# Kernel optimization log

Hardware: AMD Instinct MI355X
Metric: run time of the kernel (lower is better)

## Reference

```python
import jax, jax.numpy as jnp
import numpy as np

IN_DIMS = (32, 64, 96, 128)
N_EXPERTS = len(IN_DIMS)
MAX_F = max(IN_DIMS)
D = 2 * MAX_F
N = 8192
TOP_K = 2
H_DIM = 1024
OUT_DIM = 768
LN_EPS = 1e-6


def _build_mask():
    # mask[f] = [1]*s + [0]*(MAX_F-s) + [1]*s + [0]*(MAX_F-s), shape (E, 1, D)
    m = np.zeros((N_EXPERTS, 1, D), dtype=np.float32)
    for i, s in enumerate(IN_DIMS):
        m[i, 0, :s] = 1.0
        m[i, 0, MAX_F:MAX_F + s] = 1.0
    return jnp.asarray(m)

_MASK = _build_mask()


def _multi_in_expert(x_final, expert_weights, expert_indices, W, b):
    """MoE dispatch/combine of MultiInSizeLinear (expert_indices path).
    x_final: (E, N, D); expert_weights/indices: (N, K); W: (E, O, D); b: (E, O)."""
    Wm = W * _MASK                                   # (E, O, D) masked per-size weights
    # per-expert outputs for every token (the torch loop computes these per mask group)
    Y = jnp.einsum('end,eod->eno', x_final, Wm) + b[:, None, :]   # (E, N, O)
    valid = expert_indices < N_EXPERTS               # (N, K) real-expert mask
    rsum = jnp.sum(expert_weights * valid, axis=-1, keepdims=True)
    rsum = jnp.where(rsum == 0, 1.0, rsum)
    wnorm = jnp.where(valid, expert_weights / rsum, 0.0)          # (N, K)
    safe = jnp.where(valid, expert_indices, 0)
    n_idx = jnp.arange(Y.shape[1])
    gathered = Y[safe, n_idx[:, None]]               # (N, K, O)
    return jnp.sum(wnorm[..., None] * gathered, axis=1)           # (N, O)


def setup_inputs() -> dict:
    key = jax.random.key(0)
    ks = jax.random.split(key, 12)
    s_hid = 1.0 / np.sqrt(D)
    s_out = 1.0 / np.sqrt(H_DIM)
    return {
        'x': jax.random.normal(ks[0], (N, D), jnp.float32),
        'in_feat_size': jax.random.randint(ks[1], (N,), 0, MAX_F, jnp.int64) if jax.config.jax_enable_x64 else jax.random.randint(ks[1], (N,), 0, MAX_F, jnp.int32),
        'expert_weights': jax.random.uniform(ks[2], (N, TOP_K), jnp.float32),
        'expert_indices': jax.random.randint(ks[3], (N, TOP_K), 0, 6, jnp.int32),
        'x_final': jax.random.normal(ks[4], (N_EXPERTS, N, D), jnp.float32),
        'W_hid': jax.random.normal(ks[5], (N_EXPERTS, H_DIM, D), jnp.float32) * s_hid,
        'b_hid': jax.random.normal(ks[6], (N_EXPERTS, H_DIM), jnp.float32) * s_hid,
        'W_out': jax.random.normal(ks[7], (OUT_DIM, H_DIM), jnp.float32) * s_out,
        'b_out': jax.random.normal(ks[8], (OUT_DIM,), jnp.float32) * s_out,
        'W_res': jax.random.normal(ks[9], (N_EXPERTS, OUT_DIM, D), jnp.float32) * s_hid,
        'b_res': jax.random.normal(ks[10], (N_EXPERTS, OUT_DIM), jnp.float32) * s_hid,
        'ln_w': jnp.ones((OUT_DIM,), jnp.float32),
    }


def reference(x, in_feat_size, expert_weights, expert_indices, x_final,
              W_hid, b_hid, W_out, b_out, W_res, b_res, ln_w):
    xf = jnp.nan_to_num(x_final, nan=0.0)
    hid = _multi_in_expert(xf, expert_weights, expert_indices, W_hid, b_hid)
    hid = jax.nn.gelu(hid, approximate=False)
    out = hid @ W_out.T + b_out                      # output_layer (dropout p=0 -> identity)
    res = _multi_in_expert(xf, expert_weights, expert_indices, W_res, b_res)
    out = out + res
    # T5LayerNorm (RMSNorm)
    var = jnp.mean(out * out, axis=-1, keepdims=True)
    return ln_w * (out * jax.lax.rsqrt(var + LN_EPS))
```

## Files before the change

kernel.cpp:

```cpp
#include <hip/hip_runtime.h>
#include <hip/hip_bf16.h>

#define TOKENS 8192
#define D_IN   256
#define HDIM   1024
#define ODIM   768
#define KPACK  704
#define NCHUNK 88

typedef short bf16x8 __attribute__((ext_vector_type(8)));
typedef float f32x4  __attribute__((ext_vector_type(4)));

static __device__ __forceinline__ ushort f2b(float f) {
    union { __hip_bfloat16 b; ushort u; } cv;
    cv.b = __float2bfloat16(f);
    return cv.u;
}
static __device__ __forceinline__ float b2f(ushort u) {
    union { ushort u; __hip_bfloat16 b; } cv;
    cv.u = u;
    return __bfloat162float(cv.b);
}

static __device__ __forceinline__ void chunk_map(int c8, int& e, int& d0) {
    int cc;
    if (c8 < 8)       { e = 0; cc = c8; }
    else if (c8 < 24) { e = 1; cc = c8 - 8; }
    else if (c8 < 48) { e = 2; cc = c8 - 24; }
    else              { e = 3; cc = c8 - 48; }
    int half = 4 * (e + 1);
    d0 = (cc < half) ? cc * 8 : 128 + (cc - half) * 8;
}

static __device__ __forceinline__ void stage16(const ushort* g, ushort* l) {
    __builtin_amdgcn_global_load_lds(
        (const __attribute__((address_space(1))) void*)g,
        (__attribute__((address_space(3))) void*)l, 16, 0, 0);
}

static __device__ __forceinline__ float gelu_f(float v) {
    float y = 0.7978845608f * v * (1.f + 0.044715f * v * v);
    return v - v / (__expf(2.f * y) + 1.f);
}

#define A_ITEMS  (TOKENS * NCHUNK)
#define B_ITEMS  (1792 * NCHUNK)
#define W_ITEMS  (768 * 128)
__global__ __launch_bounds__(256) void k_pack(
    const float* __restrict__ ew, const int* __restrict__ ei,
    const float* __restrict__ xf,
    const float* __restrict__ Whid, const float* __restrict__ bhid,
    const float* __restrict__ Wres, const float* __restrict__ bres,
    const float* __restrict__ Wout,
    ushort* __restrict__ Ap, ushort* __restrict__ Bp, ushort* __restrict__ Wb) {
    int gid = blockIdx.x * 256 + threadIdx.x;
    if (gid < A_ITEMS) {
        int n  = gid / NCHUNK;
        int c8 = gid - n * NCHUNK;
        int   i0 = ei[2 * n], i1 = ei[2 * n + 1];
        float w0 = ew[2 * n], w1 = ew[2 * n + 1];
        bool v0 = (unsigned)i0 < 4u, v1 = (unsigned)i1 < 4u;
        float rs = (v0 ? w0 : 0.f) + (v1 ? w1 : 0.f);
        if (rs == 0.f) rs = 1.f;
        float o0 = v0 ? w0 / rs : 0.f;
        float o1 = v1 ? w1 / rs : 0.f;
        ushort o[8] __attribute__((aligned(16))) = {0, 0, 0, 0, 0, 0, 0, 0};
        if (c8 < 80) {
            int e, d0;
            chunk_map(c8, e, d0);
            float w = ((v0 && i0 == e) ? o0 : 0.f) + ((v1 && i1 == e) ? o1 : 0.f);
            if (w != 0.f) {
                const float* s = xf + ((size_t)e * TOKENS + n) * D_IN + d0;
#pragma unroll
                for (int j = 0; j < 8; ++j) {
                    float v = s[j];
                    if (!(v == v)) v = 0.f;
                    o[j] = f2b(w * v);
                }
            }
        } else if (c8 == 80) {
#pragma unroll
            for (int j = 0; j < 4; ++j) {
                float m = ((v0 && i0 == j) ? o0 : 0.f) + ((v1 && i1 == j) ? o1 : 0.f);
                o[j] = f2b(m);
            }
        }
        *(uint4*)(Ap + (size_t)n * KPACK + c8 * 8) = *(const uint4*)o;
    } else if (gid < A_ITEMS + B_ITEMS) {
        int g2 = gid - A_ITEMS;
        int o_ = g2 / NCHUNK;
        int c8 = g2 - o_ * NCHUNK;
        ushort v[8] __attribute__((aligned(16))) = {0, 0, 0, 0, 0, 0, 0, 0};
        if (c8 < 80) {
            int e, d0;
            chunk_map(c8, e, d0);
            const float* s = (o_ < HDIM)
                ? Whid + ((size_t)e * HDIM + o_) * D_IN + d0
                : Wres + ((size_t)e * ODIM + (o_ - HDIM)) * D_IN + d0;
#pragma unroll
            for (int j = 0; j < 8; ++j) v[j] = f2b(s[j]);
        } else if (c8 == 80) {
#pragma unroll
            for (int j = 0; j < 4; ++j) {
                float b = (o_ < HDIM) ? bhid[j * HDIM + o_] : bres[j * ODIM + (o_ - HDIM)];
                v[j] = f2b(b);
            }
        }
        *(uint4*)(Bp + (size_t)o_ * KPACK + c8 * 8) = *(const uint4*)v;
    } else {
        int g3 = gid - A_ITEMS - B_ITEMS;
        const float* s = Wout + (size_t)g3 * 8;
        ushort v[8] __attribute__((aligned(16)));
#pragma unroll
        for (int j = 0; j < 8; ++j) v[j] = f2b(s[j]);
        *(uint4*)(Wb + (size_t)g3 * 8) = *(const uint4*)v;
    }
}

__global__ __launch_bounds__(256, 2) void k_gemm1(
    const ushort* __restrict__ A, const ushort* __restrict__ B,
    ushort* __restrict__ hidB, ushort* __restrict__ resb) {
    __shared__ __align__(16) ushort As[2][128 * 64];
    __shared__ __align__(16) ushort Bs[2][128 * 64];
    const int tid = threadIdx.x;
    const int lane = tid & 63, w = tid >> 6;
    const int wr = w >> 1, wc = w & 1;
    const int r = lane & 15, g = lane >> 4;
    const int sx = r & 7;

    int bid  = blockIdx.x;
    int widx = (bid & 7) * 112 + (bid >> 3);
    int bm = widx / 14, bn = widx - bm * 14;

    const int srow = tid >> 3;
    const int gc   = (tid & 7) ^ (srow & 7);
    const ushort* Ag = A + (size_t)(bm * 128 + srow) * KPACK + gc * 8;
    const ushort* Bg = B + (size_t)(bn * 128 + srow) * KPACK + gc * 8;
    const int ldst = (w * 8) * 64;

#define G1_STAGE(p, kt) do {                                            \
    _Pragma("unroll")                                                   \
    for (int i_ = 0; i_ < 4; ++i_) {                                    \
        stage16(Ag + (size_t)(i_ * 32) * KPACK + (kt), &As[p][ldst + i_ * 32 * 64]); \
        stage16(Bg + (size_t)(i_ * 32) * KPACK + (kt), &Bs[p][ldst + i_ * 32 * 64]); \
    } } while (0)

    G1_STAGE(0, 0);
    G1_STAGE(1, 64);

    f32x4 acc[4][4] = {};
    const int cA = (wr * 64 + r) * 64;
    const int cB = (wc * 64 + r) * 64;
    const int cs0 = ((0 * 4 + g) ^ sx) * 8;
    const int cs1 = ((1 * 4 + g) ^ sx) * 8;

    int cur = 0;
#pragma unroll
    for (int t = 0; t < 11; ++t) {
        if (t < 10) asm volatile("s_waitcnt vmcnt(8)" ::: "memory");
        else        asm volatile("s_waitcnt vmcnt(0)" ::: "memory");
        __builtin_amdgcn_s_barrier();
        const ushort* Ab = As[cur];
        const ushort* Bb = Bs[cur];
        bf16x8 a0[4], b0[4], a1[4], b1[4];
#pragma unroll
        for (int jj = 0; jj < 4; ++jj) {
            b0[jj] = *(const bf16x8*)&Bb[cB + jj * 16 * 64 + cs0];
            b1[jj] = *(const bf16x8*)&Bb[cB + jj * 16 * 64 + cs1];
        }
#pragma unroll
        for (int i = 0; i < 4; ++i) {
            a0[i] = *(const bf16x8*)&Ab[cA + i * 16 * 64 + cs0];
            a1[i] = *(const bf16x8*)&Ab[cA + i * 16 * 64 + cs1];
        }
        asm volatile("s_waitcnt lgkmcnt(0)" ::: "memory");
        __builtin_amdgcn_sched_barrier(0);
        __builtin_amdgcn_s_barrier();
        if (t + 2 < 11) G1_STAGE(cur, (t + 2) * 64);
        __builtin_amdgcn_s_setprio(1);
#pragma unroll
        for (int i = 0; i < 4; ++i)
#pragma unroll
            for (int jj = 0; jj < 4; ++jj)
                acc[i][jj] = __builtin_amdgcn_mfma_f32_16x16x32_bf16(
                    a0[i], b0[jj], acc[i][jj], 0, 0, 0);
#pragma unroll
        for (int i = 0; i < 4; ++i)
#pragma unroll
            for (int jj = 0; jj < 4; ++jj)
                acc[i][jj] = __builtin_amdgcn_mfma_f32_16x16x32_bf16(
                    a1[i], b1[jj], acc[i][jj], 0, 0, 0);
        __builtin_amdgcn_s_setprio(0);
        cur ^= 1;
    }
#undef G1_STAGE

    if (bn < 8) {
#pragma unroll
        for (int fi = 0; fi < 4; ++fi) {
#pragma unroll
            for (int jj = 0; jj < 4; ++jj) {
                int col = bn * 128 + wc * 64 + jj * 16 + r;
#pragma unroll
                for (int qq = 0; qq < 4; ++qq) {
                    int row = bm * 128 + wr * 64 + fi * 16 + g * 4 + qq;
                    hidB[(size_t)row * HDIM + col] = f2b(gelu_f(acc[fi][jj][qq]));
                }
            }
        }
    } else {
#pragma unroll
        for (int fi = 0; fi < 4; ++fi) {
#pragma unroll
            for (int jj = 0; jj < 4; ++jj) {
                int col = (bn - 8) * 128 + wc * 64 + jj * 16 + r;
#pragma unroll
                for (int qq = 0; qq < 4; ++qq) {
                    int row = bm * 128 + wr * 64 + fi * 16 + g * 4 + qq;
                    resb[(size_t)row * ODIM + col] = f2b(acc[fi][jj][qq]);
                }
            }
        }
    }
}

__global__ __launch_bounds__(256, 2) void k_gemm2(
    const ushort* __restrict__ A, const ushort* __restrict__ B,
    const float* __restrict__ bout, const ushort* __restrict__ resb,
    ushort* __restrict__ outb) {
    __shared__ __align__(16) ushort As[2][128 * 64];
    __shared__ __align__(16) ushort Bs[2][128 * 64];
    const int tid = threadIdx.x;
    const int lane = tid & 63, w = tid >> 6;
    const int wr = w >> 1, wc = w & 1;
    const int r = lane & 15, g = lane >> 4;

    int bid  = blockIdx.x;
    int widx = (bid & 7) * 48 + (bid >> 3);
    int bm = widx / 6, bn = widx - bm * 6;

    const int srow = tid >> 3;
    const int gc   = (tid & 7) ^ (srow & 7);
    const ushort* Ag = A + (size_t)(bm * 128 + srow) * HDIM + gc * 8;
    const ushort* Bg = B + (size_t)(bn * 128 + srow) * HDIM + gc * 8;
    const int ldst = (w * 8) * 64;

#define G2_STAGE(p, kt) do {                                            \
    _Pragma("unroll")                                                   \
    for (int i_ = 0; i_ < 4; ++i_) {                                    \
        stage16(Ag + (size_t)(i_ * 32) * HDIM + (kt), &As[p][ldst + i_ * 32 * 64]); \
        stage16(Bg + (size_t)(i_ * 32) * HDIM + (kt), &Bs[p][ldst + i_ * 32 * 64]); \
    } } while (0)

    G2_STAGE(0, 0);
    G2_STAGE(1, 64);

    f32x4 acc[4][4] = {};
    const int cA = (wr * 64 + r) * 64;
    const int cB = (wc * 64 + r) * 64;
    const int sx = r & 7;
    const int cs0 = ((0 * 4 + g) ^ sx) * 8;
    const int cs1 = ((1 * 4 + g) ^ sx) * 8;

    int cur = 0;
#pragma unroll
    for (int t = 0; t < 16; ++t) {
        if (t < 15) asm volatile("s_waitcnt vmcnt(8)" ::: "memory");
        else        asm volatile("s_waitcnt vmcnt(0)" ::: "memory");
        __builtin_amdgcn_s_barrier();
        const ushort* Ab = As[cur];
        const ushort* Bb = Bs[cur];
        bf16x8 a0[4], b0[4], a1[4], b1[4];
#pragma unroll
        for (int jj = 0; jj < 4; ++jj) {
            b0[jj] = *(const bf16x8*)&Bb[cB + jj * 16 * 64 + cs0];
            b1[jj] = *(const bf16x8*)&Bb[cB + jj * 16 * 64 + cs1];
        }
#pragma unroll
        for (int i = 0; i < 4; ++i) {
            a0[i] = *(const bf16x8*)&Ab[cA + i * 16 * 64 + cs0];
            a1[i] = *(const bf16x8*)&Ab[cA + i * 16 * 64 + cs1];
        }
        asm volatile("s_waitcnt lgkmcnt(0)" ::: "memory");
        __builtin_amdgcn_sched_barrier(0);
        __builtin_amdgcn_s_barrier();
        if (t + 2 < 16) G2_STAGE(cur, (t + 2) * 64);
        __builtin_amdgcn_s_setprio(1);
#pragma unroll
        for (int i = 0; i < 4; ++i)
#pragma unroll
            for (int jj = 0; jj < 4; ++jj)
                acc[i][jj] = __builtin_amdgcn_mfma_f32_16x16x32_bf16(
                    a0[i], b0[jj], acc[i][jj], 0, 0, 0);
#pragma unroll
        for (int i = 0; i < 4; ++i)
#pragma unroll
            for (int jj = 0; jj < 4; ++jj)
                acc[i][jj] = __builtin_amdgcn_mfma_f32_16x16x32_bf16(
                    a1[i], b1[jj], acc[i][jj], 0, 0, 0);
        __builtin_amdgcn_s_setprio(0);
        cur ^= 1;
    }
#undef G2_STAGE

#pragma unroll
    for (int fi = 0; fi < 4; ++fi) {
#pragma unroll
        for (int jj = 0; jj < 4; ++jj) {
            int col = bn * 128 + wc * 64 + jj * 16 + r;
#pragma unroll
            for (int qq = 0; qq < 4; ++qq) {
                int row = bm * 128 + wr * 64 + fi * 16 + g * 4 + qq;
                size_t idx = (size_t)row * ODIM + col;
                float v = acc[fi][jj][qq] + bout[col] + b2f(resb[idx]);
                outb[idx] = f2b(v);
            }
        }
    }
}

__global__ __launch_bounds__(256) void k_rms(
    const ushort* __restrict__ outb, const float* __restrict__ lnw,
    float* __restrict__ out) {
    int t = threadIdx.x;
    int lr = t >> 5, lc = t & 31;
    int row = blockIdx.x * 8 + lr;
    const ushort* p = outb + (size_t)row * ODIM;
    float v[24];
    float s = 0.f;
#pragma unroll
    for (int c = 0; c < 3; ++c) {
        uint4 q = *(const uint4*)(p + (lc + 32 * c) * 8);
        const ushort* u = (const ushort*)&q;
#pragma unroll
        for (int k = 0; k < 8; ++k) {
            float f = b2f(u[k]);
            v[c * 8 + k] = f;
            s += f * f;
        }
    }
#pragma unroll
    for (int off = 16; off > 0; off >>= 1) s += __shfl_xor(s, off, 32);
    float sc = rsqrtf(s * (1.f / 768.f) + 1e-6f);
    float* o = out + (size_t)row * ODIM;
#pragma unroll
    for (int c = 0; c < 3; ++c) {
        int base = (lc + 32 * c) * 8;
        float4 l0 = *(const float4*)&lnw[base];
        float4 l1 = *(const float4*)&lnw[base + 4];
        float4 w0, w1;
        w0.x = l0.x * v[c * 8 + 0] * sc;
        w0.y = l0.y * v[c * 8 + 1] * sc;
        w0.z = l0.z * v[c * 8 + 2] * sc;
        w0.w = l0.w * v[c * 8 + 3] * sc;
        w1.x = l1.x * v[c * 8 + 4] * sc;
        w1.y = l1.y * v[c * 8 + 5] * sc;
        w1.z = l1.z * v[c * 8 + 6] * sc;
        w1.w = l1.w * v[c * 8 + 7] * sc;
        *(float4*)&o[base]     = w0;
        *(float4*)&o[base + 4] = w1;
    }
}

extern "C" void kernel_launch(void* const* d_in, const int* in_sizes, int n_in,
                              void* d_out, int out_size, void* d_ws, size_t ws_size,
                              hipStream_t stream) {
    const float* ew   = (const float*)d_in[2];
    const int*   ei   = (const int*)d_in[3];
    const float* xf   = (const float*)d_in[4];
    const float* Whid = (const float*)d_in[5];
    const float* bhid = (const float*)d_in[6];
    const float* Wout = (const float*)d_in[7];
    const float* bout = (const float*)d_in[8];
    const float* Wres = (const float*)d_in[9];
    const float* bres = (const float*)d_in[10];
    const float* lnw  = (const float*)d_in[11];

    char* ws = (char*)d_ws;
    ushort* Ap   = (ushort*)(ws);
    ushort* Bp   = (ushort*)(ws + 11534336);
    ushort* Wb   = (ushort*)(ws + 14057472);
    ushort* hidB = (ushort*)(ws + 15630336);
    ushort* resb = (ushort*)(ws + 32407552);
    ushort* outb = (ushort*)(ws + 44990464);

    k_pack<<<3816, 256, 0, stream>>>(ew, ei, xf, Whid, bhid, Wres, bres, Wout,
                                     Ap, Bp, Wb);
    k_gemm1<<<896, 256, 0, stream>>>(Ap, Bp, hidB, resb);
    k_gemm2<<<384, 256, 0, stream>>>(hidB, Wb, bout, resb, outb);
    k_rms<<<1024, 256, 0, stream>>>(outb, lnw, (float*)d_out);
}
```

Before: 68.02 us.

## Widen gemm1 output tile to 128x256 with 32-wide K steps

The first GEMM now uses a 128x256 block tile instead of 128x128, halving the grid to 448 blocks. K steps shrink from 64 to 32 (22 iterations), with a new LDS layout and XOR swizzle, and each wave holds 4x8 accumulators. The aim is more reuse of each A-tile load across more output columns and less global traffic per FLOP. The cost is more accumulator registers and fewer blocks, which may hurt occupancy and tail balance on the 256-CU device.

```diff
diff --git a/kernel.cpp b/kernel.cpp
--- a/kernel.cpp
+++ b/kernel.cpp
@@ -120,87 +120,74 @@
 __global__ __launch_bounds__(256, 2) void k_gemm1(
     const ushort* __restrict__ A, const ushort* __restrict__ B,
     ushort* __restrict__ hidB, ushort* __restrict__ resb) {
-    __shared__ __align__(16) ushort As[2][128 * 64];
-    __shared__ __align__(16) ushort Bs[2][128 * 64];
+    __shared__ __align__(16) ushort As[2][128 * 32];
+    __shared__ __align__(16) ushort Bs[2][256 * 32];
     const int tid = threadIdx.x;
     const int lane = tid & 63, w = tid >> 6;
     const int wr = w >> 1, wc = w & 1;
     const int r = lane & 15, g = lane >> 4;
-    const int sx = r & 7;
 
     int bid  = blockIdx.x;
-    int widx = (bid & 7) * 112 + (bid >> 3);
-    int bm = widx / 14, bn = widx - bm * 14;
-
-    const int srow = tid >> 3;
-    const int gc   = (tid & 7) ^ (srow & 7);
+    int widx = (bid & 7) * 56 + (bid >> 3);
+    int bm = widx / 7, bn = widx - bm * 7;
+
+    const int srow = tid >> 2;
+    const int gc   = (tid & 3) ^ ((srow >> 1) & 3);
     const ushort* Ag = A + (size_t)(bm * 128 + srow) * KPACK + gc * 8;
-    const ushort* Bg = B + (size_t)(bn * 128 + srow) * KPACK + gc * 8;
-    const int ldst = (w * 8) * 64;
-
-#define G1_STAGE(p, kt) do {                                            \
-    _Pragma("unroll")                                                   \
-    for (int i_ = 0; i_ < 4; ++i_) {                                    \
-        stage16(Ag + (size_t)(i_ * 32) * KPACK + (kt), &As[p][ldst + i_ * 32 * 64]); \
-        stage16(Bg + (size_t)(i_ * 32) * KPACK + (kt), &Bs[p][ldst + i_ * 32 * 64]); \
-    } } while (0)
+    const ushort* Bg = B + (size_t)(bn * 256 + srow) * KPACK + gc * 8;
+    const int ldst = (w * 16) * 32;
+
+#define G1_STAGE(p, kt) do {                                                 \
+    stage16(Ag + (kt),                        &As[p][ldst]);                 \
+    stage16(Ag + (size_t)64 * KPACK + (kt),   &As[p][64 * 32 + ldst]);       \
+    _Pragma("unroll")                                                        \
+    for (int i_ = 0; i_ < 4; ++i_)                                           \
+        stage16(Bg + (size_t)(i_ * 64) * KPACK + (kt),                       \
+                &Bs[p][i_ * 64 * 32 + ldst]); } while (0)
 
     G1_STAGE(0, 0);
-    G1_STAGE(1, 64);
-
-    f32x4 acc[4][4] = {};
-    const int cA = (wr * 64 + r) * 64;
-    const int cB = (wc * 64 + r) * 64;
-    const int cs0 = ((0 * 4 + g) ^ sx) * 8;
-    const int cs1 = ((1 * 4 + g) ^ sx) * 8;
+    G1_STAGE(1, 32);
+
+    f32x4 acc[4][8] = {};
+    const int cA = (wr * 64 + r) * 32;
+    const int cB = (wc * 128 + r) * 32;
+    const int cs = (g ^ ((r >> 1) & 3)) * 8;
 
     int cur = 0;
 #pragma unroll
-    for (int t = 0; t < 11; ++t) {
-        if (t < 10) asm volatile("s_waitcnt vmcnt(8)" ::: "memory");
+    for (int t = 0; t < 22; ++t) {
+        if (t < 21) asm volatile("s_waitcnt vmcnt(6)" ::: "memory");
         else        asm volatile("s_waitcnt vmcnt(0)" ::: "memory");
         __builtin_amdgcn_s_barrier();
         const ushort* Ab = As[cur];
         const ushort* Bb = Bs[cur];
-        bf16x8 a0[4], b0[4], a1[4], b1[4];
-#pragma unroll
-        for (int jj = 0; jj < 4; ++jj) {
-            b0[jj] = *(const bf16x8*)&Bb[cB + jj * 16 * 64 + cs0];
-            b1[jj] = *(const bf16x8*)&Bb[cB + jj * 16 * 64 + cs1];
-        }
-#pragma unroll
-        for (int i = 0; i < 4; ++i) {
-            a0[i] = *(const bf16x8*)&Ab[cA + i * 16 * 64 + cs0];
-            a1[i] = *(const bf16x8*)&Ab[cA + i * 16 * 64 + cs1];
-        }
+        bf16x8 af[4], bf_[8];
+#pragma unroll
+        for (int j = 0; j < 8; ++j) bf_[j] = *(const bf16x8*)&Bb[cB + j * 16 * 32 + cs];
+#pragma unroll
+        for (int i = 0; i < 4; ++i) af[i] = *(const bf16x8*)&Ab[cA + i * 16 * 32 + cs];
         asm volatile("s_waitcnt lgkmcnt(0)" ::: "memory");
         __builtin_amdgcn_sched_barrier(0);
         __builtin_amdgcn_s_barrier();
-        if (t + 2 < 11) G1_STAGE(cur, (t + 2) * 64);
+        if (t + 2 < 22) G1_STAGE(cur, (t + 2) * 32);
         __builtin_amdgcn_s_setprio(1);
 #pragma unroll
         for (int i = 0; i < 4; ++i)
 #pragma unroll
-            for (int jj = 0; jj < 4; ++jj)
-                acc[i][jj] = __builtin_amdgcn_mfma_f32_16x16x32_bf16(
-                    a0[i], b0[jj], acc[i][jj], 0, 0, 0);
-#pragma unroll
-        for (int i = 0; i < 4; ++i)
-#pragma unroll
-            for (int jj = 0; jj < 4; ++jj)
-                acc[i][jj] = __builtin_amdgcn_mfma_f32_16x16x32_bf16(
-                    a1[i], b1[jj], acc[i][jj], 0, 0, 0);
+            for (int j = 0; j < 8; ++j)
+                acc[i][j] = __builtin_amdgcn_mfma_f32_16x16x32_bf16(
+                    af[i], bf_[j], acc[i][j], 0, 0, 0);
         __builtin_amdgcn_s_setprio(0);
         cur ^= 1;
     }
 #undef G1_STAGE
 
-    if (bn < 8) {
+    if (bn < 4) {
 #pragma unroll
         for (int fi = 0; fi < 4; ++fi) {
 #pragma unroll
-            for (int jj = 0; jj < 4; ++jj) {
-                int col = bn * 128 + wc * 64 + jj * 16 + r;
+            for (int jj = 0; jj < 8; ++jj) {
+                int col = bn * 256 + wc * 128 + jj * 16 + r;
 #pragma unroll
                 for (int qq = 0; qq < 4; ++qq) {
                     int row = bm * 128 + wr * 64 + fi * 16 + g * 4 + qq;
@@ -212,8 +199,8 @@
 #pragma unroll
         for (int fi = 0; fi < 4; ++fi) {
 #pragma unroll
-            for (int jj = 0; jj < 4; ++jj) {
-                int col = (bn - 8) * 128 + wc * 64 + jj * 16 + r;
+            for (int jj = 0; jj < 8; ++jj) {
+                int col = (bn - 4) * 256 + wc * 128 + jj * 16 + r;
 #pragma unroll
                 for (int qq = 0; qq < 4; ++qq) {
                     int row = bm * 128 + wr * 64 + fi * 16 + g * 4 + qq;
@@ -386,7 +373,7 @@
 
     k_pack<<<3816, 256, 0, stream>>>(ew, ei, xf, Whid, bhid, Wres, bres, Wout,
                                      Ap, Bp, Wb);
-    k_gemm1<<<896, 256, 0, stream>>>(Ap, Bp, hidB, resb);
+    k_gemm1<<<448, 256, 0, stream>>>(Ap, Bp, hidB, resb);
     k_gemm2<<<384, 256, 0, stream>>>(hidB, Wb, bout, resb, outb);
     k_rms<<<1024, 256, 0, stream>>>(outb, lnw, (float*)d_out);
 }
```

After: 70.22 us (median of 2 runs). +3.2%, slower.
